# Kernel optimization log

Hardware: AMD Instinct MI355X
Metric: run time of the kernel (lower is better)

Reference implementation:

```python
import jax, jax.numpy as jnp
import numpy as np

N = 16777216  # rows
G = 1024      # distinct group keys (power of 2 -> no binary-search padding)


def setup_inputs() -> dict:
    key = jax.random.key(0)
    k1, k2, k3 = jax.random.split(key, 3)
    # guarantee every group id in [0, G) appears at least once
    base = jnp.arange(G, dtype=jnp.int32)
    rest = jax.random.randint(k1, (N - G,), 0, G, dtype=jnp.int32)
    key_col = jax.random.permutation(k2, jnp.concatenate([base, rest])).reshape(-1, 1)
    val_col = jax.random.normal(k3, (N, 1), dtype=jnp.float32)
    return {"key_col": key_col, "val_col": val_col}


def _group_indices(x_flat, uniq_desc):
    # Faithful vectorized replication of find_mapping_indices: binary search of each
    # x against the reverse-sorted (descending) unique keys. G is a power of 2 so
    # N_prime == G and no front padding occurs.
    steps = int(np.log2(G))
    offset = G // 2
    pos = (x_flat <= uniq_desc[offset]).astype(jnp.int32) * offset
    offset = offset // 2  # int(ceil(offset/2)) == offset//2 for powers of two
    for _ in range(1, steps):
        bins = (x_flat <= uniq_desc[pos + offset]).astype(jnp.int32)
        pos = pos + bins * offset
        offset = offset // 2
    return pos  # [N] group index in [0, G)


def reference(key_col, val_col):
    x = key_col.reshape(-1)
    v = val_col.reshape(-1)
    # torch.sort(torch.unique(x), descending=True): all G values present by construction
    uniq_desc = jnp.unique(x, size=G)[::-1]
    gid = _group_indices(x, uniq_desc)
    # fused segmented reduces replace the per-group masked_select loop (same math)
    s = jax.ops.segment_sum(v, gid, num_segments=G)
    cnt = jax.ops.segment_sum(jnp.ones_like(v), gid, num_segments=G)
    avg = s / cnt  # torch.mean per group; every group non-empty
    mn = jax.ops.segment_min(v, gid, num_segments=G)
    mx = jax.ops.segment_max(v, gid, num_segments=G)
    # group_selection_mask is all-True (every group occupied) -> masked_select is identity
    key_out = uniq_desc.reshape(-1, 1)
    return (key_out,
            s.reshape(-1, 1),
            avg.reshape(-1, 1),
            mn.reshape(-1, 1),
            mx.reshape(-1, 1))
```

## Files before the change

kernel.cpp:

```cpp
#include <hip/hip_runtime.h>

#define G 1024
#define SCALE_S 4096.0f
#define BCNT_SHIFT 24
#define BELEM_BIAS (1 << 15)
#define BLOW_MASK ((1u << BCNT_SHIFT) - 1)
#define GCNT_SHIFT 44
#define GSUM_BIAS (1ll << 23)
#define GLOW_MASK ((1ULL << GCNT_SHIFT) - 1)
#define NREP 8

__device__ __forceinline__ unsigned omap(float x) {
    unsigned u = __float_as_uint(x);
    return (u & 0x80000000u) ? ~u : (u | 0x80000000u);
}
__device__ __forceinline__ float ounmap(unsigned o) {
    unsigned u = (o & 0x80000000u) ? (o & 0x7fffffffu) : ~o;
    return __uint_as_float(u);
}

__global__ __launch_bounds__(256) void gb_warm(
    const int4* __restrict__ keys, const float4* __restrict__ vals, int n4w,
    unsigned* __restrict__ rmaxo, unsigned* __restrict__ rminv)
{
    __shared__ unsigned s_mn[G];
    __shared__ unsigned s_mx[G];
    for (int k = threadIdx.x; k < G; k += 256) { s_mn[k] = 0xffffffffu; s_mx[k] = 0u; }
    __syncthreads();

    const int stride = gridDim.x * 256;
    for (int i = blockIdx.x * 256 + threadIdx.x; i < n4w; i += stride) {
        int4 k4 = keys[i]; float4 v4 = vals[i];
        unsigned o;
        o = omap(v4.x); atomicMin(&s_mn[k4.x], o); atomicMax(&s_mx[k4.x], o);
        o = omap(v4.y); atomicMin(&s_mn[k4.y], o); atomicMax(&s_mx[k4.y], o);
        o = omap(v4.z); atomicMin(&s_mn[k4.z], o); atomicMax(&s_mx[k4.z], o);
        o = omap(v4.w); atomicMin(&s_mn[k4.w], o); atomicMax(&s_mx[k4.w], o);
    }
    __syncthreads();

    const int r = blockIdx.x & (NREP - 1);
    for (int k = threadIdx.x; k < G; k += 256) {
        const unsigned mn = s_mn[k], mx = s_mx[k];
        if (mn != 0xffffffffu) atomicMax(&rminv[r * G + k], ~mn);
        if (mx != 0u)          atomicMax(&rmaxo[r * G + k], mx);
    }
}

__global__ __launch_bounds__(1024) void gb_gate(
    const unsigned* __restrict__ rmaxo, const unsigned* __restrict__ rminv,
    unsigned* __restrict__ gate2)
{
    const int k = threadIdx.x;
    unsigned mx = 0u, mv = 0u;
    for (int r = 0; r < NREP; ++r) {
        mx = max(mx, rmaxo[r * G + k]);
        mv = max(mv, rminv[r * G + k]);
    }
    __shared__ unsigned l_tmin[1024];
    __shared__ unsigned l_tmax[1024];
    l_tmin[k] = ~mv;
    l_tmax[k] = mx;
    __syncthreads();
    for (int s = 512; s > 0; s >>= 1) {
        if (k < s) {
            l_tmin[k] = max(l_tmin[k], l_tmin[k + s]);
            l_tmax[k] = min(l_tmax[k], l_tmax[k + s]);
        }
        __syncthreads();
    }
    if (k == 0) { gate2[0] = l_tmin[0]; gate2[1] = l_tmax[0]; }
}

__global__ __launch_bounds__(256) void gb_main(
    const int4* __restrict__ keys, const float4* __restrict__ vals, int n4,
    unsigned long long* __restrict__ racc,
    unsigned* __restrict__ rmaxo, unsigned* __restrict__ rminv,
    const unsigned* __restrict__ gate2)
{
    __shared__ unsigned s_sc[G];
    __shared__ unsigned s_mn[G];
    __shared__ unsigned s_mx[G];
    for (int k = threadIdx.x; k < G; k += 256) {
        s_sc[k] = 0u; s_mn[k] = 0xffffffffu; s_mx[k] = 0u;
    }
    const unsigned Tmin = gate2[0];
    const unsigned Tmax = gate2[1];
    __syncthreads();

#define MAIN_ELEM(KK, VV)                                                      \
        {                                                                      \
            const int k = (KK); const float v = (VV);                          \
            const unsigned o = omap(v);                                        \
            if (o <= Tmin) atomicMin(&s_mn[k], o);                             \
            if (o >= Tmax) atomicMax(&s_mx[k], o);                             \
            const int vf = __float2int_rn(v * SCALE_S);                        \
            atomicAdd(&s_sc[k], (1u << BCNT_SHIFT) + (unsigned)(vf + BELEM_BIAS)); \
        }

    const int stride = gridDim.x * 256;
    int i = blockIdx.x * 256 + threadIdx.x;
    if (i < n4) {
        int4 k4 = keys[i]; float4 v4 = vals[i];
        for (i += stride; ; i += stride) {
            const bool more = (i < n4);
            int4 nk; float4 nv;
            if (more) { nk = keys[i]; nv = vals[i]; }
            MAIN_ELEM(k4.x, v4.x) MAIN_ELEM(k4.y, v4.y)
            MAIN_ELEM(k4.z, v4.z) MAIN_ELEM(k4.w, v4.w)
            if (!more) break;
            k4 = nk; v4 = nv;
        }
    }
#undef MAIN_ELEM
    __syncthreads();

    const int r = blockIdx.x & (NREP - 1);
    for (int k = threadIdx.x; k < G; k += 256) {
        const unsigned c = s_sc[k];
        if (c) {
            const unsigned n = c >> BCNT_SHIFT;
            const long long s = (long long)(c & BLOW_MASK) - ((long long)n << 15);
            atomicAdd(&racc[r * G + k],
                      ((unsigned long long)n << GCNT_SHIFT) +
                      (unsigned long long)(s + (long long)n * GSUM_BIAS));
        }
        const unsigned mn = s_mn[k], mx = s_mx[k];
        if (mn != 0xffffffffu) atomicMax(&rminv[r * G + k], ~mn);
        if (mx != 0u)          atomicMax(&rmaxo[r * G + k], mx);
    }
}

__global__ __launch_bounds__(256) void gb_write(
    const unsigned long long* __restrict__ racc,
    const unsigned* __restrict__ rmaxo, const unsigned* __restrict__ rminv,
    float* __restrict__ out)
{
    const int k = blockIdx.x * 256 + threadIdx.x;
    unsigned long long cell = 0ull; unsigned mx = 0u, mv = 0u;
    for (int r = 0; r < NREP; ++r) {
        cell += racc[r * G + k];
        mx = max(mx, rmaxo[r * G + k]);
        mv = max(mv, rminv[r * G + k]);
    }
    const unsigned n = (unsigned)(cell >> GCNT_SHIFT);
    const long long s = (long long)(cell & GLOW_MASK) - (long long)n * GSUM_BIAS;
    const float sum = (float)((double)s * (1.0 / (double)SCALE_S));
    const int g = (G - 1) - k;
    out[g]         = (float)k;
    out[G + g]     = sum;
    out[2 * G + g] = sum / (float)n;
    out[3 * G + g] = ounmap(~mv);
    out[4 * G + g] = ounmap(mx);
}

extern "C" void kernel_launch(void* const* d_in, const int* in_sizes, int n_in,
                              void* d_out, int out_size, void* d_ws, size_t ws_size,
                              hipStream_t stream) {
    const int4*   keys = (const int4*)d_in[0];
    const float4* vals = (const float4*)d_in[1];
    const int n   = in_sizes[0];
    const int n4  = n / 4;
    int n4w = n4 >> 5;
    if (n4w < 1)  n4w = (n4 < 1) ? 0 : n4;
    if (n4w > n4) n4w = n4;

    unsigned long long* racc  = (unsigned long long*)d_ws;
    unsigned*           rmaxo = (unsigned*)(racc + NREP * G);
    unsigned*           rminv = rmaxo + NREP * G;
    unsigned*           gate2 = rminv + NREP * G;
    const size_t acc_bytes = (size_t)NREP * G * (8 + 4 + 4) + 2 * sizeof(unsigned);

    hipMemsetAsync(d_ws, 0, acc_bytes, stream);

    hipLaunchKernelGGL(gb_warm, dim3(512), dim3(256), 0, stream,
                       keys, vals, n4w, rmaxo, rminv);
    hipLaunchKernelGGL(gb_gate, dim3(1), dim3(1024), 0, stream,
                       rmaxo, rminv, gate2);
    hipLaunchKernelGGL(gb_main, dim3(2048), dim3(256), 0, stream,
                       keys, vals, n4, racc, rmaxo, rminv, gate2);
    hipLaunchKernelGGL(gb_write, dim3(G / 256), dim3(256), 0, stream,
                       racc, rmaxo, rminv, (float*)d_out);
}
```

Before: 170.2 us.

## Widen shared sum accumulators to 64-bit and push gated min/max directly to global

The per-block shared min/max tables are removed. Values passing the gate thresholds now do atomicMax directly on global replicated arrays, which cuts LDS atomics per element from three to one. The shared sum+count cell becomes 64-bit with a finer fixed-point scale (2^20), which improves precision but makes each LDS atomic 64-bit. The global sum replicas increase from 8 to 64, and the warm-up sample doubles so the gate thresholds are tighter. The risk is that global atomics from elements passing the gate add latency if the gate lets through more values than expected.

```diff
diff --git a/kernel.cpp b/kernel.cpp
--- a/kernel.cpp
+++ b/kernel.cpp
@@ -1,14 +1,15 @@
 #include <hip/hip_runtime.h>
 
 #define G 1024
-#define SCALE_S 4096.0f
-#define BCNT_SHIFT 24
-#define BELEM_BIAS (1 << 15)
-#define BLOW_MASK ((1u << BCNT_SHIFT) - 1)
+#define SCALEF 1048576.0f
+#define CNT_SHIFT 42
+#define ELEM_BIAS (1 << 24)
+#define LOW_MASK ((1ULL << CNT_SHIFT) - 1)
 #define GCNT_SHIFT 44
 #define GSUM_BIAS (1ll << 23)
 #define GLOW_MASK ((1ULL << GCNT_SHIFT) - 1)
-#define NREP 8
+#define NREP 64
+#define NREP_MM 8
 
 __device__ __forceinline__ unsigned omap(float x) {
     unsigned u = __float_as_uint(x);
@@ -39,7 +40,7 @@
     }
     __syncthreads();
 
-    const int r = blockIdx.x & (NREP - 1);
+    const int r = blockIdx.x & (NREP_MM - 1);
     for (int k = threadIdx.x; k < G; k += 256) {
         const unsigned mn = s_mn[k], mx = s_mx[k];
         if (mn != 0xffffffffu) atomicMax(&rminv[r * G + k], ~mn);
@@ -53,7 +54,7 @@
 {
     const int k = threadIdx.x;
     unsigned mx = 0u, mv = 0u;
-    for (int r = 0; r < NREP; ++r) {
+    for (int r = 0; r < NREP_MM; ++r) {
         mx = max(mx, rmaxo[r * G + k]);
         mv = max(mv, rminv[r * G + k]);
     }
@@ -78,24 +79,26 @@
     unsigned* __restrict__ rmaxo, unsigned* __restrict__ rminv,
     const unsigned* __restrict__ gate2)
 {
-    __shared__ unsigned s_sc[G];
-    __shared__ unsigned s_mn[G];
-    __shared__ unsigned s_mx[G];
-    for (int k = threadIdx.x; k < G; k += 256) {
-        s_sc[k] = 0u; s_mn[k] = 0xffffffffu; s_mx[k] = 0u;
-    }
+    __shared__ unsigned long long s_sc[G];
+    for (int k = threadIdx.x; k < G; k += 256) s_sc[k] = 0ull;
+
     const unsigned Tmin = gate2[0];
     const unsigned Tmax = gate2[1];
     __syncthreads();
+
+    const int rmm = blockIdx.x & (NREP_MM - 1);
+    unsigned* __restrict__ rmaxo_r = rmaxo + rmm * G;
+    unsigned* __restrict__ rminv_r = rminv + rmm * G;
 
 #define MAIN_ELEM(KK, VV)                                                      \
         {                                                                      \
             const int k = (KK); const float v = (VV);                          \
             const unsigned o = omap(v);                                        \
-            if (o <= Tmin) atomicMin(&s_mn[k], o);                             \
-            if (o >= Tmax) atomicMax(&s_mx[k], o);                             \
-            const int vf = __float2int_rn(v * SCALE_S);                        \
-            atomicAdd(&s_sc[k], (1u << BCNT_SHIFT) + (unsigned)(vf + BELEM_BIAS)); \
+            if (o <= Tmin) atomicMax(&rminv_r[k], ~o);                         \
+            if (o >= Tmax) atomicMax(&rmaxo_r[k], o);                          \
+            const int vf = __float2int_rn(v * SCALEF);                         \
+            atomicAdd(&s_sc[k], (1ULL << CNT_SHIFT) +                          \
+                      (unsigned long long)(unsigned)(vf + ELEM_BIAS));         \
         }
 
     const int stride = gridDim.x * 256;
@@ -116,18 +119,16 @@
     __syncthreads();
 
     const int r = blockIdx.x & (NREP - 1);
+    unsigned long long* __restrict__ racc_r = racc + r * G;
     for (int k = threadIdx.x; k < G; k += 256) {
-        const unsigned c = s_sc[k];
-        if (c) {
-            const unsigned n = c >> BCNT_SHIFT;
-            const long long s = (long long)(c & BLOW_MASK) - ((long long)n << 15);
-            atomicAdd(&racc[r * G + k],
+        const unsigned long long cell = s_sc[k];
+        const unsigned n = (unsigned)(cell >> CNT_SHIFT);
+        if (n) {
+            const long long s = (long long)(cell & LOW_MASK) - ((long long)n << 24);
+            atomicAdd(&racc_r[k],
                       ((unsigned long long)n << GCNT_SHIFT) +
                       (unsigned long long)(s + (long long)n * GSUM_BIAS));
         }
-        const unsigned mn = s_mn[k], mx = s_mx[k];
-        if (mn != 0xffffffffu) atomicMax(&rminv[r * G + k], ~mn);
-        if (mx != 0u)          atomicMax(&rmaxo[r * G + k], mx);
     }
 }
 
@@ -137,15 +138,16 @@
     float* __restrict__ out)
 {
     const int k = blockIdx.x * 256 + threadIdx.x;
-    unsigned long long cell = 0ull; unsigned mx = 0u, mv = 0u;
-    for (int r = 0; r < NREP; ++r) {
-        cell += racc[r * G + k];
+    unsigned long long cell = 0ull;
+    for (int r = 0; r < NREP; ++r) cell += racc[r * G + k];
+    unsigned mx = 0u, mv = 0u;
+    for (int r = 0; r < NREP_MM; ++r) {
         mx = max(mx, rmaxo[r * G + k]);
         mv = max(mv, rminv[r * G + k]);
     }
     const unsigned n = (unsigned)(cell >> GCNT_SHIFT);
     const long long s = (long long)(cell & GLOW_MASK) - (long long)n * GSUM_BIAS;
-    const float sum = (float)((double)s * (1.0 / (double)SCALE_S));
+    const float sum = (float)((double)s * (1.0 / (double)SCALEF));
     const int g = (G - 1) - k;
     out[g]         = (float)k;
     out[G + g]     = sum;
@@ -161,15 +163,16 @@
     const float4* vals = (const float4*)d_in[1];
     const int n   = in_sizes[0];
     const int n4  = n / 4;
-    int n4w = n4 >> 5;
+    int n4w = n4 >> 4;
     if (n4w < 1)  n4w = (n4 < 1) ? 0 : n4;
     if (n4w > n4) n4w = n4;
 
     unsigned long long* racc  = (unsigned long long*)d_ws;
-    unsigned*           rmaxo = (unsigned*)(racc + NREP * G);
-    unsigned*           rminv = rmaxo + NREP * G;
-    unsigned*           gate2 = rminv + NREP * G;
-    const size_t acc_bytes = (size_t)NREP * G * (8 + 4 + 4) + 2 * sizeof(unsigned);
+    unsigned*           rmaxo = (unsigned*)(racc + (size_t)NREP * G);
+    unsigned*           rminv = rmaxo + (size_t)NREP_MM * G;
+    unsigned*           gate2 = rminv + (size_t)NREP_MM * G;
+    const size_t acc_bytes = (size_t)NREP * G * 8 + (size_t)NREP_MM * G * 8
+                           + 2 * sizeof(unsigned);
 
     hipMemsetAsync(d_ws, 0, acc_bytes, stream);
 
```

Result: no change. 167.1 us (-1.8%).
